# Kernel optimization log

Hardware: AMD Instinct MI355X
Metric: run time of the kernel (lower is better)

Reference implementation:

```python
import jax, jax.numpy as jnp
import numpy as np
from jax import lax

X_DIM, Z_DIM, H_DIM, G_DIM, I_DIM = 1, 16, 16, 8, 16
T_LEN, BATCH = 512, 2048


def _lin_params(key, fan_in, fan_out):
    k1, k2 = jax.random.split(key)
    bound = 1.0 / np.sqrt(fan_in)
    W = jax.random.uniform(k1, (fan_out, fan_in), jnp.float32, -bound, bound)
    b = jax.random.uniform(k2, (fan_out,), jnp.float32, -bound, bound)
    return W, b


def setup_inputs() -> dict:
    key = jax.random.key(0)
    ks = jax.random.split(key, 12)
    x = jax.random.normal(ks[0], (T_LEN, BATCH, X_DIM), jnp.float32)
    eps_z = jax.random.normal(ks[1], (T_LEN, BATCH, Z_DIM), jnp.float32)
    # LSTM (pytorch layout: gates i,f,g,o stacked)
    bnd = 1.0 / np.sqrt(H_DIM)
    lstm_Wih = jax.random.uniform(ks[2], (4 * H_DIM, X_DIM), jnp.float32, -bnd, bnd)
    lstm_Whh = jax.random.uniform(ks[3], (4 * H_DIM, H_DIM), jnp.float32, -bnd, bnd)
    lstm_bih = jax.random.uniform(ks[4], (4 * H_DIM,), jnp.float32, -bnd, bnd)
    lstm_bhh = jax.random.uniform(ks[5], (4 * H_DIM,), jnp.float32, -bnd, bnd)
    comb_W1, comb_b1 = _lin_params(ks[6], Z_DIM + H_DIM, I_DIM)
    comb_W2, comb_b2 = _lin_params(jax.random.fold_in(ks[6], 1), I_DIM, G_DIM)
    enc_W1, enc_b1 = _lin_params(ks[7], G_DIM, I_DIM)
    enc_W2, enc_b2 = _lin_params(jax.random.fold_in(ks[7], 1), I_DIM, 2 * Z_DIM)
    dec_W1, dec_b1 = _lin_params(ks[8], Z_DIM, I_DIM)
    dec_W2, dec_b2 = _lin_params(jax.random.fold_in(ks[8], 1), I_DIM, 2 * X_DIM)
    tr_W1, tr_b1 = _lin_params(ks[9], Z_DIM, I_DIM)
    tr_W2, tr_b2 = _lin_params(jax.random.fold_in(ks[9], 1), I_DIM, 2 * Z_DIM)
    return dict(x=x, eps_z=eps_z,
                lstm_Wih=lstm_Wih, lstm_Whh=lstm_Whh, lstm_bih=lstm_bih, lstm_bhh=lstm_bhh,
                comb_W1=comb_W1, comb_b1=comb_b1, comb_W2=comb_W2, comb_b2=comb_b2,
                enc_W1=enc_W1, enc_b1=enc_b1, enc_W2=enc_W2, enc_b2=enc_b2,
                dec_W1=dec_W1, dec_b1=dec_b1, dec_W2=dec_W2, dec_b2=dec_b2,
                tr_W1=tr_W1, tr_b1=tr_b1, tr_W2=tr_W2, tr_b2=tr_b2)


def _dkf_forward(x, eps_z, lstm_Wih, lstm_Whh, lstm_bih, lstm_bhh,
                 comb_W1, comb_b1, comb_W2, comb_b2,
                 enc_W1, enc_b1, enc_W2, enc_b2,
                 dec_W1, dec_b1, dec_W2, dec_b2,
                 tr_W1, tr_b1, tr_W2, tr_b2):
    T, B, _ = x.shape
    H = lstm_Whh.shape[1]
    Z = eps_z.shape[-1]

    # ---- backward LSTM: run over time-reversed x, then reverse outputs ----
    def lstm_step(carry, xt):
        h, c = carry
        gates = xt @ lstm_Wih.T + lstm_bih + h @ lstm_Whh.T + lstm_bhh  # (B, 4H)
        i, f, g, o = jnp.split(gates, 4, axis=-1)
        c = jax.nn.sigmoid(f) * c + jax.nn.sigmoid(i) * jnp.tanh(g)
        h = jax.nn.sigmoid(o) * jnp.tanh(c)
        return (h, c), h

    h0 = jnp.zeros((B, H), x.dtype)
    c0 = jnp.zeros((B, H), x.dtype)
    _, hs = lax.scan(lstm_step, (h0, c0), x[::-1])
    h_seq = hs[::-1]  # (T, B, H)

    # ---- DKF inference loop: combiner -> encoder -> reparam sample ----
    def dkf_step(z_prev, inp):
        h_t, eps_t = inp
        hz = jnp.concatenate([h_t, z_prev], axis=-1)                 # (B, H+Z)
        g = jnp.tanh(hz @ comb_W1.T + comb_b1) @ comb_W2.T + comb_b2  # (B, G)
        e = jnp.tanh(g @ enc_W1.T + enc_b1) @ enc_W2.T + enc_b2       # (B, 2Z)
        mu_z, logvar_z = e[:, :Z], e[:, Z:]
        z = mu_z + eps_t * jnp.exp(0.5 * logvar_z)
        return z, (z, mu_z, logvar_z, z_prev)

    z0 = jnp.zeros((B, Z), x.dtype)
    _, (z_seq, mu_z, logvar_z, z_prev_seq) = lax.scan(dkf_step, z0, (h_seq, eps_z))

    # ---- decoder p(x|z) over the whole sequence ----
    d = jnp.tanh(z_seq @ dec_W1.T + dec_b1) @ dec_W2.T + dec_b2  # (T, B, 2*X)
    Xd = d.shape[-1] // 2
    mu_x, logvar_x = d[..., :Xd], d[..., Xd:]

    # ---- latent transition prior p(z_t | z_{t-1}) ----
    tr = jnp.tanh(z_prev_seq @ tr_W1.T + tr_b1) @ tr_W2.T + tr_b2  # (T, B, 2Z)
    mu_tr, logvar_tr = tr[..., :Z], tr[..., Z:]

    # single packed output: (T, B, 2*X + 4*Z)
    return jnp.concatenate([mu_x, logvar_x, mu_z, logvar_z, mu_tr, logvar_tr], axis=-1)


def reference(x, eps_z, lstm_Wih, lstm_Whh, lstm_bih, lstm_bhh,
              comb_W1, comb_b1, comb_W2, comb_b2,
              enc_W1, enc_b1, enc_W2, enc_b2,
              dec_W1, dec_b1, dec_W2, dec_b2,
              tr_W1, tr_b1, tr_W2, tr_b2):
    return _dkf_forward(x, eps_z, lstm_Wih, lstm_Whh, lstm_bih, lstm_bhh,
                        comb_W1, comb_b1, comb_W2, comb_b2,
                        enc_W1, enc_b1, enc_W2, enc_b2,
                        dec_W1, dec_b1, dec_W2, dec_b2,
                        tr_W1, tr_b1, tr_W2, tr_b2)
```

## Files before the change

kernel.cpp:

```cpp
#include <hip/hip_runtime.h>

#define T_LEN 512
#define BATCH 2048
#define OUTW  66

typedef unsigned int u32;
typedef short v8s __attribute__((ext_vector_type(8)));
typedef float v4f __attribute__((ext_vector_type(4)));
typedef float v2f __attribute__((ext_vector_type(2)));
typedef u32   v2u __attribute__((ext_vector_type(2)));

union FragU { v8s s; u32 w[4]; };

__device__ __forceinline__ float fexp2(float x){ return __builtin_amdgcn_exp2f(x); }
__device__ __forceinline__ float frcp (float x){ return __builtin_amdgcn_rcpf(x); }
__device__ __forceinline__ float ftanh(float x){
    return fmaf(2.f, frcp(1.f + fexp2(-2.88539008f * x)), -1.f);
}
__device__ __forceinline__ float fsig(float x){
    return frcp(1.f + fexp2(-1.44269504f * x));
}
__device__ __forceinline__ u32 cvtpk(float lo, float hi){
    u32 r; asm("v_cvt_pk_bf16_f32 %0, %1, %2" : "=v"(r) : "v"(lo), "v"(hi)); return r;
}
__device__ __forceinline__ float ubf_lo(u32 w){ union{u32 i; float f;} v; v.i = w << 16;         return v.f; }
__device__ __forceinline__ float ubf_hi(u32 w){ union{u32 i; float f;} v; v.i = w & 0xffff0000u; return v.f; }
__device__ __forceinline__ void pswap32(u32& a, u32& b){
    asm("v_permlane32_swap_b32 %0, %1" : "+v"(a), "+v"(b));
}
__device__ __forceinline__ void pswap16(u32& a, u32& b){
    asm("v_permlane16_swap_b32 %0, %1" : "+v"(a), "+v"(b));
}
#define MFMA(A,B,C) __builtin_amdgcn_mfma_f32_16x16x32_bf16((A),(B),(C),0,0,0)

__device__ __forceinline__ void pack4(v4f d, u32& Ah, u32& Bh, u32& Al, u32& Bl){
    Ah = cvtpk(d[0], d[1]);
    Bh = cvtpk(d[2], d[3]);
    Al = cvtpk(d[0] - ubf_lo(Ah), d[1] - ubf_hi(Ah));
    Bl = cvtpk(d[2] - ubf_lo(Bh), d[3] - ubf_hi(Bh));
}
__device__ __forceinline__ v8s swizB(u32 Ah, u32 Bh, u32 Al, u32 Bl){
    pswap32(Ah, Al); pswap16(Ah, Al);
    pswap32(Bh, Bl); pswap16(Bh, Bl);
    FragU F; F.w[0] = Ah; F.w[1] = Bh; F.w[2] = Al; F.w[3] = Bl;
    return F.s;
}
__device__ __forceinline__ v8s reB(v4f d){
    u32 Ah, Bh, Al, Bl; pack4(d, Ah, Bh, Al, Bl);
    return swizB(Ah, Bh, Al, Bl);
}
__device__ __forceinline__ void loadAsplit(const float* W, int ld, int R, int C,
                                           v8s& A1, v8s& A2){
    const int r = threadIdx.x & 15, G = threadIdx.x >> 4;
    const int g2 = G & 1;
    FragU H, L;
#pragma unroll
    for (int p = 0; p < 4; ++p){
        const int k0 = 8*g2 + 2*p;
        const float a = (r < R && k0     < C) ? W[r*ld + k0]     : 0.f;
        const float b = (r < R && k0 + 1 < C) ? W[r*ld + k0 + 1] : 0.f;
        const u32 h = cvtpk(a, b);
        const u32 l = cvtpk(a - ubf_lo(h), b - ubf_hi(h));
        H.w[p] = h;
        L.w[p] = (G < 2) ? l : 0u;
    }
    A1 = H.s; A2 = L.s;
}
__device__ __forceinline__ v8s loadA1(const float* W, int ld, int R, int C){
    const int r = threadIdx.x & 15, G = threadIdx.x >> 4;
    const int g2 = G & 1;
    FragU H;
#pragma unroll
    for (int p = 0; p < 4; ++p){
        const int k0 = 8*g2 + 2*p;
        const float a = (r < R && k0     < C) ? W[r*ld + k0]     : 0.f;
        const float b = (r < R && k0 + 1 < C) ? W[r*ld + k0 + 1] : 0.f;
        H.w[p] = cvtpk(a, b);
    }
    return H.s;
}
__device__ __forceinline__ v4f loadCbias(const float* bsrc, int R){
    const int m = threadIdx.x >> 4;
    v4f c;
#pragma unroll
    for (int j = 0; j < 4; ++j){
        const int idx = 4*m + j;
        c[j] = (idx < R) ? bsrc[idx] : 0.f;
    }
    return c;
}
__device__ __forceinline__ v4f tanh4(v4f a){
    v4f r;
#pragma unroll
    for (int j = 0; j < 4; ++j) r[j] = ftanh(a[j]);
    return r;
}
__device__ __forceinline__ void st2(float* p, float a, float b){
    v2f v; v[0] = a; v[1] = b; *(v2f*)p = v;
}
__device__ __forceinline__ v8s loadHfrag(const float* out, int t, int bc, int G){
    const float* o = out + (size_t)(t*BATCH + bc) * OUTW;
    FragU F;
    v2u a = *(const v2u*)(o + 34 + 4*G);
    v2u b = *(const v2u*)(o + 36 + 4*G);
    F.w[0] = a[0]; F.w[1] = a[1]; F.w[2] = b[0]; F.w[3] = b[1];
    return F.s;
}

__global__ __launch_bounds__(64)
void dkf_mfma_kernel(const float* __restrict__ x,   const float* __restrict__ eps_z,
                     const float* __restrict__ Wih, const float* __restrict__ Whh,
                     const float* __restrict__ bih, const float* __restrict__ bhh,
                     const float* __restrict__ cW1, const float* __restrict__ cb1,
                     const float* __restrict__ cW2, const float* __restrict__ cb2,
                     const float* __restrict__ eW1, const float* __restrict__ eb1,
                     const float* __restrict__ eW2, const float* __restrict__ eb2,
                     const float* __restrict__ dW1, const float* __restrict__ db1,
                     const float* __restrict__ dW2, const float* __restrict__ db2,
                     const float* __restrict__ tW1, const float* __restrict__ tb1,
                     const float* __restrict__ tW2, const float* __restrict__ tb2,
                     float* __restrict__ out)
{
    const int lane = threadIdx.x;
    const int c    = lane & 15;
    const int G    = lane >> 4;
    const int bc   = blockIdx.x * 16 + c;

    {
        v8s A1g[4], A2g[4];
#pragma unroll
        for (int g = 0; g < 4; ++g)
            loadAsplit(Whh + 256*g, 16, 16, 16, A1g[g], A2g[g]);
        v4f bc4[4];
#pragma unroll
        for (int g = 0; g < 4; ++g){
            v4f t;
#pragma unroll
            for (int j = 0; j < 4; ++j){
                const int idx = 16*g + 4*G + j;
                t[j] = bih[idx] + bhh[idx];
            }
            bc4[g] = t;
        }
        float wihr[4][4];
#pragma unroll
        for (int g = 0; g < 4; ++g)
#pragma unroll
            for (int j = 0; j < 4; ++j) wihr[g][j] = Wih[16*g + 4*G + j];

        v4f cst = {0.f, 0.f, 0.f, 0.f};
        FragU Z0; Z0.w[0]=Z0.w[1]=Z0.w[2]=Z0.w[3]=0u;
        v8s hb = Z0.s;
        float xv[2];
        xv[0] = x[(T_LEN-1)*BATCH + bc];
        xv[1] = x[(T_LEN-2)*BATCH + bc];

        for (int t2 = 0; t2 < T_LEN/2; ++t2){
#pragma unroll
            for (int q = 0; q < 2; ++q){
                const int t = T_LEN - 1 - 2*t2 - q;
                v4f ci, cf, cg, co;
#pragma unroll
                for (int j = 0; j < 4; ++j){
                    ci[j] = fmaf(wihr[0][j], xv[q], bc4[0][j]);
                    cf[j] = fmaf(wihr[1][j], xv[q], bc4[1][j]);
                    cg[j] = fmaf(wihr[2][j], xv[q], bc4[2][j]);
                    co[j] = fmaf(wihr[3][j], xv[q], bc4[3][j]);
                }
                v4f di  = MFMA(A1g[0], hb, ci); di  = MFMA(A2g[0], hb, di);
                v4f df  = MFMA(A1g[1], hb, cf); df  = MFMA(A2g[1], hb, df);
                v4f dg  = MFMA(A1g[2], hb, cg); dg  = MFMA(A2g[2], hb, dg);
                v4f doo = MFMA(A1g[3], hb, co); doo = MFMA(A2g[3], hb, doo);
                v4f hv;
#pragma unroll
                for (int j = 0; j < 4; ++j){
                    const float si = fsig(di[j]);
                    const float sf = fsig(df[j]);
                    const float tg = ftanh(dg[j]);
                    const float so = fsig(doo[j]);
                    cst[j] = fmaf(sf, cst[j], si * tg);
                    hv[j]  = so * ftanh(cst[j]);
                }
                u32 Ah, Bh, Al, Bl;
                pack4(hv, Ah, Bh, Al, Bl);
                {
                    float* o = out + (size_t)(t*BATCH + bc) * OUTW;
                    v2u sh; sh[0] = Ah; sh[1] = Bh;
                    v2u sl; sl[0] = Al; sl[1] = Bl;
                    *(v2u*)(o + 34 + 2*G) = sh;
                    *(v2u*)(o + 42 + 2*G) = sl;
                }
                hb = swizB(Ah, Bh, Al, Bl);
                const int tn = (t >= 2) ? (t - 2) : 0;
                xv[q] = x[tn*BATCH + bc];
            }
        }
    }

    __threadfence();

    v8s C1h1, C1h2; loadAsplit(cW1,       32, 16, 16, C1h1, C1h2);
    v8s C1z1, C1z2; loadAsplit(cW1 + 16,  32, 16, 16, C1z1, C1z2);
    v8s C21,  C22;  loadAsplit(cW2,       16,  8, 16, C21,  C22);
    v8s E11,  E12;  loadAsplit(eW1,        8, 16,  8, E11,  E12);
    v8s E2m1, E2m2; loadAsplit(eW2,       16, 16, 16, E2m1, E2m2);
    v8s E2v1, E2v2; loadAsplit(eW2 + 256, 16, 16, 16, E2v1, E2v2);
    v8s D1  = loadA1(dW1,       16, 16, 16);
    v8s D2  = loadA1(dW2,       16,  2, 16);
    v8s T1  = loadA1(tW1,       16, 16, 16);
    v8s T2m = loadA1(tW2,       16, 16, 16);
    v8s T2v = loadA1(tW2 + 256, 16, 16, 16);
    const v4f bC1  = loadCbias(cb1, 16);
    const v4f bC2  = loadCbias(cb2,  8);
    const v4f bE1  = loadCbias(eb1, 16);
    const v4f bE2m = loadCbias(eb2, 16);
    const v4f bE2v = loadCbias(eb2 + 16, 16);
    const v4f bD1  = loadCbias(db1, 16);
    const v4f bD2  = loadCbias(db2,  2);
    const v4f bT1  = loadCbias(tb1, 16);
    const v4f bT2m = loadCbias(tb2, 16);
    const v4f bT2v = loadCbias(tb2 + 16, 16);

    FragU Z1; Z1.w[0]=Z1.w[1]=Z1.w[2]=Z1.w[3]=0u;
    v8s zb = Z1.s;

    v8s hbr[2];
    v4f epr[2];
    hbr[0] = loadHfrag(out, 0, bc, G);
    hbr[1] = loadHfrag(out, 1, bc, G);
    epr[0] = *(const v4f*)(eps_z + (size_t)(0*BATCH + bc)*16 + 4*G);
    epr[1] = *(const v4f*)(eps_z + (size_t)(1*BATCH + bc)*16 + 4*G);

    for (int t2 = 0; t2 < T_LEN/2; ++t2){
#pragma unroll
        for (int q = 0; q < 2; ++q){
            const int t = 2*t2 + q;
            float* o = out + (size_t)(t*BATCH + bc) * OUTW;
            const v8s hb = hbr[q];
            const v4f ep = epr[q];
            {
                int tn = t + 2; if (tn >= T_LEN) tn = T_LEN - 1;
                hbr[q] = loadHfrag(out, tn, bc, G);
                epr[q] = *(const v4f*)(eps_z + (size_t)(tn*BATCH + bc)*16 + 4*G);
            }
            v4f dt1 = MFMA(T1, zb, bT1);
            v4f at  = tanh4(dt1);
            v8s atb = reB(at);
            v4f dmt = MFMA(T2m, atb, bT2m);
            v4f dlt = MFMA(T2v, atb, bT2v);
            v4f d1 = MFMA(C1h1, hb, bC1);
            d1 = MFMA(C1h2, hb, d1);
            d1 = MFMA(C1z1, zb, d1);
            d1 = MFMA(C1z2, zb, d1);
            v4f a1  = tanh4(d1);
            v8s a1b = reB(a1);
            v4f d2 = MFMA(C21, a1b, bC2); d2 = MFMA(C22, a1b, d2);
            v8s gb2 = reB(d2);
            v4f d3 = MFMA(E11, gb2, bE1); d3 = MFMA(E12, gb2, d3);
            v4f e1  = tanh4(d3);
            v8s e1b = reB(e1);
            v4f dmu = MFMA(E2m1, e1b, bE2m); dmu = MFMA(E2m2, e1b, dmu);
            v4f dlv = MFMA(E2v1, e1b, bE2v); dlv = MFMA(E2v2, e1b, dlv);
            v4f zv;
#pragma unroll
            for (int j = 0; j < 4; ++j){
                const float s = fexp2(0.72134752f * fminf(dlv[j], 40.f));
                zv[j] = fmaf(ep[j], s, dmu[j]);
            }
            zb = reB(zv);
            v4f dd1 = MFMA(D1, zb, bD1);
            v4f ad  = tanh4(dd1);
            v8s adb = reB(ad);
            v4f dd2 = MFMA(D2, adb, bD2);
            st2(o +  2 + 4*G, dmu[0], dmu[1]); st2(o +  4 + 4*G, dmu[2], dmu[3]);
            st2(o + 18 + 4*G, dlv[0], dlv[1]); st2(o + 20 + 4*G, dlv[2], dlv[3]);
            st2(o + 34 + 4*G, dmt[0], dmt[1]); st2(o + 36 + 4*G, dmt[2], dmt[3]);
            st2(o + 50 + 4*G, dlt[0], dlt[1]); st2(o + 52 + 4*G, dlt[2], dlt[3]);
            if (lane < 16) st2(o, dd2[0], dd2[1]);
        }
    }
}

extern "C" void kernel_launch(void* const* d_in, const int* in_sizes, int n_in,
                              void* d_out, int out_size, void* d_ws, size_t ws_size,
                              hipStream_t stream) {
    (void)in_sizes; (void)n_in; (void)out_size; (void)d_ws; (void)ws_size;
    const float* x     = (const float*)d_in[0];
    const float* eps_z = (const float*)d_in[1];
    const float* Wih   = (const float*)d_in[2];
    const float* Whh   = (const float*)d_in[3];
    const float* bih   = (const float*)d_in[4];
    const float* bhh   = (const float*)d_in[5];
    const float* cW1   = (const float*)d_in[6];
    const float* cb1   = (const float*)d_in[7];
    const float* cW2   = (const float*)d_in[8];
    const float* cb2   = (const float*)d_in[9];
    const float* eW1   = (const float*)d_in[10];
    const float* eb1   = (const float*)d_in[11];
    const float* eW2   = (const float*)d_in[12];
    const float* eb2   = (const float*)d_in[13];
    const float* dW1   = (const float*)d_in[14];
    const float* db1   = (const float*)d_in[15];
    const float* dW2   = (const float*)d_in[16];
    const float* db2   = (const float*)d_in[17];
    const float* tW1   = (const float*)d_in[18];
    const float* tb1   = (const float*)d_in[19];
    const float* tW2   = (const float*)d_in[20];
    const float* tb2   = (const float*)d_in[21];

    dkf_mfma_kernel<<<BATCH/16, 64, 0, stream>>>(
        x, eps_z, Wih, Whh, bih, bhh,
        cW1, cb1, cW2, cb2, eW1, eb1, eW2, eb2,
        dW1, db1, dW2, db2, tW1, tb1, tW2, tb2,
        (float*)d_out);
}
```

Before: 1.004 ms.

## Fold comb/enc linear layers, split MFMA chains, and pipeline the DKF step off the critical path

Folds the comb second layer and enc first layer into one precomputed 16x16 matrix and bias, since no nonlinearity sits between them, which removes two MFMAs from the serial chain. The hi/lo bf16 split MFMAs now run as independent accumulations that are summed afterwards, shortening dependent MFMA chains in both the LSTM and DKF loops. The h-dependent part of the comb layer is computed one step ahead, and the transition and decoder MLPs for z_{t-1} run at the start of the next step, overlapping them with the critical path. It also unrolls by four with deeper prefetch and sets launch bounds to one block. The algebraic fold changes rounding slightly, and the extra live registers raise register pressure.

New measurement: 927.3 us. 7.6% less time.

```diff
diff --git a/kernel.cpp b/kernel.cpp
--- a/kernel.cpp
+++ b/kernel.cpp
@@ -79,6 +79,27 @@
     }
     return H.s;
 }
+__device__ __forceinline__ void loadMsplit(const float* eW1, const float* cW2,
+                                           v8s& A1, v8s& A2){
+    const int r = threadIdx.x & 15, G = threadIdx.x >> 4;
+    const int g2 = G & 1;
+    FragU H, L;
+#pragma unroll
+    for (int p = 0; p < 4; ++p){
+        const int k0 = 8*g2 + 2*p;
+        float a = 0.f, b = 0.f;
+#pragma unroll
+        for (int j = 0; j < 8; ++j){
+            a = fmaf(eW1[r*8 + j], cW2[j*16 + k0],     a);
+            b = fmaf(eW1[r*8 + j], cW2[j*16 + k0 + 1], b);
+        }
+        const u32 h = cvtpk(a, b);
+        const u32 l = cvtpk(a - ubf_lo(h), b - ubf_hi(h));
+        H.w[p] = h;
+        L.w[p] = (G < 2) ? l : 0u;
+    }
+    A1 = H.s; A2 = L.s;
+}
 __device__ __forceinline__ v4f loadCbias(const float* bsrc, int R){
     const int m = threadIdx.x >> 4;
     v4f c;
@@ -88,6 +109,12 @@
         c[j] = (idx < R) ? bsrc[idx] : 0.f;
     }
     return c;
+}
+__device__ __forceinline__ v4f tanh4s(v4f a, v4f b){
+    v4f r;
+#pragma unroll
+    for (int j = 0; j < 4; ++j) r[j] = ftanh(a[j] + b[j]);
+    return r;
 }
 __device__ __forceinline__ v4f tanh4(v4f a){
     v4f r;
@@ -107,7 +134,7 @@
     return F.s;
 }
 
-__global__ __launch_bounds__(64)
+__global__ __launch_bounds__(64, 1)
 void dkf_mfma_kernel(const float* __restrict__ x,   const float* __restrict__ eps_z,
                      const float* __restrict__ Wih, const float* __restrict__ Whh,
                      const float* __restrict__ bih, const float* __restrict__ bhh,
@@ -125,6 +152,7 @@
     const int c    = lane & 15;
     const int G    = lane >> 4;
     const int bc   = blockIdx.x * 16 + c;
+    const v4f z4   = {0.f, 0.f, 0.f, 0.f};
 
     {
         v8s A1g[4], A2g[4];
@@ -151,33 +179,33 @@
         v4f cst = {0.f, 0.f, 0.f, 0.f};
         FragU Z0; Z0.w[0]=Z0.w[1]=Z0.w[2]=Z0.w[3]=0u;
         v8s hb = Z0.s;
-        float xv[2];
-        xv[0] = x[(T_LEN-1)*BATCH + bc];
-        xv[1] = x[(T_LEN-2)*BATCH + bc];
-
-        for (int t2 = 0; t2 < T_LEN/2; ++t2){
-#pragma unroll
-            for (int q = 0; q < 2; ++q){
-                const int t = T_LEN - 1 - 2*t2 - q;
+        float xr[4];
+#pragma unroll
+        for (int i = 0; i < 4; ++i) xr[i] = x[(T_LEN-1-i)*BATCH + bc];
+
+        for (int t4 = 0; t4 < T_LEN/4; ++t4) {
+#pragma unroll
+            for (int q = 0; q < 4; ++q) {
+                const int t = T_LEN - 1 - 4*t4 - q;
                 v4f ci, cf, cg, co;
 #pragma unroll
                 for (int j = 0; j < 4; ++j){
-                    ci[j] = fmaf(wihr[0][j], xv[q], bc4[0][j]);
-                    cf[j] = fmaf(wihr[1][j], xv[q], bc4[1][j]);
-                    cg[j] = fmaf(wihr[2][j], xv[q], bc4[2][j]);
-                    co[j] = fmaf(wihr[3][j], xv[q], bc4[3][j]);
+                    ci[j] = fmaf(wihr[0][j], xr[q], bc4[0][j]);
+                    cf[j] = fmaf(wihr[1][j], xr[q], bc4[1][j]);
+                    cg[j] = fmaf(wihr[2][j], xr[q], bc4[2][j]);
+                    co[j] = fmaf(wihr[3][j], xr[q], bc4[3][j]);
                 }
-                v4f di  = MFMA(A1g[0], hb, ci); di  = MFMA(A2g[0], hb, di);
-                v4f df  = MFMA(A1g[1], hb, cf); df  = MFMA(A2g[1], hb, df);
-                v4f dg  = MFMA(A1g[2], hb, cg); dg  = MFMA(A2g[2], hb, dg);
-                v4f doo = MFMA(A1g[3], hb, co); doo = MFMA(A2g[3], hb, doo);
+                v4f ui  = MFMA(A1g[0], hb, ci);  v4f vi  = MFMA(A2g[0], hb, z4);
+                v4f uf  = MFMA(A1g[1], hb, cf);  v4f vf  = MFMA(A2g[1], hb, z4);
+                v4f ug  = MFMA(A1g[2], hb, cg);  v4f vg  = MFMA(A2g[2], hb, z4);
+                v4f uo  = MFMA(A1g[3], hb, co);  v4f vo  = MFMA(A2g[3], hb, z4);
                 v4f hv;
 #pragma unroll
                 for (int j = 0; j < 4; ++j){
-                    const float si = fsig(di[j]);
-                    const float sf = fsig(df[j]);
-                    const float tg = ftanh(dg[j]);
-                    const float so = fsig(doo[j]);
+                    const float si = fsig(ui[j] + vi[j]);
+                    const float sf = fsig(uf[j] + vf[j]);
+                    const float tg = ftanh(ug[j] + vg[j]);
+                    const float so = fsig(uo[j] + vo[j]);
                     cst[j] = fmaf(sf, cst[j], si * tg);
                     hv[j]  = so * ftanh(cst[j]);
                 }
@@ -191,8 +219,8 @@
                     *(v2u*)(o + 42 + 2*G) = sl;
                 }
                 hb = swizB(Ah, Bh, Al, Bl);
-                const int tn = (t >= 2) ? (t - 2) : 0;
-                xv[q] = x[tn*BATCH + bc];
+                const int tn = (t >= 4) ? (t - 4) : 0;
+                xr[q] = x[tn*BATCH + bc];
             }
         }
     }
@@ -201,8 +229,7 @@
 
     v8s C1h1, C1h2; loadAsplit(cW1,       32, 16, 16, C1h1, C1h2);
     v8s C1z1, C1z2; loadAsplit(cW1 + 16,  32, 16, 16, C1z1, C1z2);
-    v8s C21,  C22;  loadAsplit(cW2,       16,  8, 16, C21,  C22);
-    v8s E11,  E12;  loadAsplit(eW1,        8, 16,  8, E11,  E12);
+    v8s M1,   M2;   loadMsplit(eW1, cW2, M1, M2);
     v8s E2m1, E2m2; loadAsplit(eW2,       16, 16, 16, E2m1, E2m2);
     v8s E2v1, E2v2; loadAsplit(eW2 + 256, 16, 16, 16, E2v1, E2v2);
     v8s D1  = loadA1(dW1,       16, 16, 16);
@@ -211,8 +238,6 @@
     v8s T2m = loadA1(tW2,       16, 16, 16);
     v8s T2v = loadA1(tW2 + 256, 16, 16, 16);
     const v4f bC1  = loadCbias(cb1, 16);
-    const v4f bC2  = loadCbias(cb2,  8);
-    const v4f bE1  = loadCbias(eb1, 16);
     const v4f bE2m = loadCbias(eb2, 16);
     const v4f bE2v = loadCbias(eb2 + 16, 16);
     const v4f bD1  = loadCbias(db1, 16);
@@ -220,63 +245,94 @@
     const v4f bT1  = loadCbias(tb1, 16);
     const v4f bT2m = loadCbias(tb2, 16);
     const v4f bT2v = loadCbias(tb2 + 16, 16);
+    v4f bMp;
+#pragma unroll
+    for (int j = 0; j < 4; ++j){
+        const int r = 4*G + j;
+        float s = eb1[r];
+#pragma unroll
+        for (int k = 0; k < 8; ++k) s = fmaf(eW1[r*8 + k], cb2[k], s);
+        bMp[j] = s;
+    }
 
     FragU Z1; Z1.w[0]=Z1.w[1]=Z1.w[2]=Z1.w[3]=0u;
     v8s zb = Z1.s;
 
-    v8s hbr[2];
-    v4f epr[2];
-    hbr[0] = loadHfrag(out, 0, bc, G);
-    hbr[1] = loadHfrag(out, 1, bc, G);
-    epr[0] = *(const v4f*)(eps_z + (size_t)(0*BATCH + bc)*16 + 4*G);
-    epr[1] = *(const v4f*)(eps_z + (size_t)(1*BATCH + bc)*16 + 4*G);
-
-    for (int t2 = 0; t2 < T_LEN/2; ++t2){
-#pragma unroll
-        for (int q = 0; q < 2; ++q){
-            const int t = 2*t2 + q;
+    v8s hbr[4];
+    v4f epr[4];
+#pragma unroll
+    for (int i = 0; i < 4; ++i){
+        hbr[i] = loadHfrag(out, i, bc, G);
+        epr[i] = *(const v4f*)(eps_z + (size_t)(i*BATCH + bc)*16 + 4*G);
+    }
+    v4f dh = MFMA(C1h1, hbr[0], bC1);
+    dh = MFMA(C1h2, hbr[0], dh);
+
+    for (int t4 = 0; t4 < T_LEN/4; ++t4){
+#pragma unroll
+        for (int q = 0; q < 4; ++q){
+            const int t = 4*t4 + q;
             float* o = out + (size_t)(t*BATCH + bc) * OUTW;
-            const v8s hb = hbr[q];
             const v4f ep = epr[q];
+            v4f d1u = MFMA(C1z1, zb, dh);
+            v4f d1v = MFMA(C1z2, zb, z4);
+            v4f t1  = MFMA(T1, zb, bT1);
+            v4f du  = MFMA(D1, zb, bD1);
             {
-                int tn = t + 2; if (tn >= T_LEN) tn = T_LEN - 1;
+                int tn = t + 4; if (tn >= T_LEN) tn = T_LEN - 1;
                 hbr[q] = loadHfrag(out, tn, bc, G);
                 epr[q] = *(const v4f*)(eps_z + (size_t)(tn*BATCH + bc)*16 + 4*G);
             }
-            v4f dt1 = MFMA(T1, zb, bT1);
-            v4f at  = tanh4(dt1);
+            {
+                const v8s hbn = hbr[(q + 1) & 3];
+                v4f nh = MFMA(C1h1, hbn, bC1);
+                nh = MFMA(C1h2, hbn, nh);
+                dh = nh;
+            }
+            v4f at  = tanh4(t1);
+            v4f ad  = tanh4(du);
             v8s atb = reB(at);
+            v8s adb = reB(ad);
             v4f dmt = MFMA(T2m, atb, bT2m);
             v4f dlt = MFMA(T2v, atb, bT2v);
-            v4f d1 = MFMA(C1h1, hb, bC1);
-            d1 = MFMA(C1h2, hb, d1);
-            d1 = MFMA(C1z1, zb, d1);
-            d1 = MFMA(C1z2, zb, d1);
-            v4f a1  = tanh4(d1);
+            v4f dd2 = MFMA(D2, adb, bD2);
+            v4f a1  = tanh4s(d1u, d1v);
             v8s a1b = reB(a1);
-            v4f d2 = MFMA(C21, a1b, bC2); d2 = MFMA(C22, a1b, d2);
-            v8s gb2 = reB(d2);
-            v4f d3 = MFMA(E11, gb2, bE1); d3 = MFMA(E12, gb2, d3);
-            v4f e1  = tanh4(d3);
+            v4f eu  = MFMA(M1, a1b, bMp);
+            v4f ev  = MFMA(M2, a1b, z4);
+            v4f e1  = tanh4s(eu, ev);
             v8s e1b = reB(e1);
-            v4f dmu = MFMA(E2m1, e1b, bE2m); dmu = MFMA(E2m2, e1b, dmu);
-            v4f dlv = MFMA(E2v1, e1b, bE2v); dlv = MFMA(E2v2, e1b, dlv);
-            v4f zv;
+            v4f muu = MFMA(E2m1, e1b, bE2m);
+            v4f muv = MFMA(E2m2, e1b, z4);
+            v4f lvu = MFMA(E2v1, e1b, bE2v);
+            v4f lvv = MFMA(E2v2, e1b, z4);
+            v4f dmu, dlv, zv;
 #pragma unroll
             for (int j = 0; j < 4; ++j){
+                dmu[j] = muu[j] + muv[j];
+                dlv[j] = lvu[j] + lvv[j];
                 const float s = fexp2(0.72134752f * fminf(dlv[j], 40.f));
                 zv[j] = fmaf(ep[j], s, dmu[j]);
             }
             zb = reB(zv);
-            v4f dd1 = MFMA(D1, zb, bD1);
-            v4f ad  = tanh4(dd1);
-            v8s adb = reB(ad);
-            v4f dd2 = MFMA(D2, adb, bD2);
             st2(o +  2 + 4*G, dmu[0], dmu[1]); st2(o +  4 + 4*G, dmu[2], dmu[3]);
             st2(o + 18 + 4*G, dlv[0], dlv[1]); st2(o + 20 + 4*G, dlv[2], dlv[3]);
             st2(o + 34 + 4*G, dmt[0], dmt[1]); st2(o + 36 + 4*G, dmt[2], dmt[3]);
             st2(o + 50 + 4*G, dlt[0], dlt[1]); st2(o + 52 + 4*G, dlt[2], dlt[3]);
-            if (lane < 16) st2(o, dd2[0], dd2[1]);
+            if (t > 0 && lane < 16){
+                float* op = out + (size_t)((t-1)*BATCH + bc) * OUTW;
+                st2(op, dd2[0], dd2[1]);
+            }
+        }
+    }
+    {
+        v4f du  = MFMA(D1, zb, bD1);
+        v4f ad  = tanh4(du);
+        v8s adb = reB(ad);
+        v4f dd2 = MFMA(D2, adb, bD2);
+        if (lane < 16){
+            float* op = out + (size_t)((T_LEN-1)*BATCH + bc) * OUTW;
+            st2(op, dd2[0], dd2[1]);
         }
     }
 }
```
